# Kernel optimization log

Measured on AMD Instinct MI355X. Metric: run time of the kernel, lower is better.

## Reference

```python
import jax, jax.numpy as jnp
import numpy as np

D_MODEL = 128
N_HEADS = 8
D_K = D_MODEL // N_HEADS
N_NODES = 50000
N_EDGES = 800000


def setup_inputs() -> dict:
    key = jax.random.key(0)
    ks = jax.random.split(key, 8)
    X = jax.random.normal(ks[0], (N_NODES, D_MODEL), dtype=jnp.float32)
    nbr_src = jax.random.randint(ks[1], (N_EDGES,), 0, N_NODES, dtype=jnp.int32)
    nbr_dst = jax.random.randint(ks[2], (N_EDGES,), 0, N_NODES, dtype=jnp.int32)
    s = 1.0 / np.sqrt(D_MODEL)
    W_qkv = jax.random.normal(ks[3], (3 * D_MODEL, D_MODEL), dtype=jnp.float32) * s
    w_bias = jax.random.normal(ks[4], (N_HEADS, D_MODEL), dtype=jnp.float32) * s
    W_gate = jax.random.normal(ks[5], (D_MODEL, D_MODEL), dtype=jnp.float32) * s
    b_gate = jax.random.normal(ks[6], (D_MODEL,), dtype=jnp.float32) * s
    W_o = jax.random.normal(ks[7], (D_MODEL, D_MODEL), dtype=jnp.float32) * s
    return {"X": X, "W_qkv": W_qkv, "w_bias": w_bias, "W_gate": W_gate,
            "b_gate": b_gate, "W_o": W_o, "nbr_src": nbr_src,
            "nbr_dst": nbr_dst, "num_cells": N_NODES}


def segment_softmax(scores, seg, num_segments):
    # scores: [E, H], seg: [E] -> softmax over edges sharing the same seg id
    mx = jax.ops.segment_max(scores, seg, num_segments=num_segments)  # [N, H]
    mx = jnp.where(jnp.isfinite(mx), mx, -1e9)
    exp_s = jnp.exp(scores - mx[seg])
    sm = jax.ops.segment_sum(exp_s, seg, num_segments=num_segments)  # [N, H]
    return exp_s / (sm[seg] + 1e-12)


def reference(X, W_qkv, w_bias, W_gate, b_gate, W_o, nbr_src, nbr_dst, num_cells):
    H, dk = N_HEADS, D_K
    scale = 1.0 / np.sqrt(dk)
    qkv = (X @ W_qkv.T).reshape(-1, 3, H, dk)      # [N, 3, H, dk]
    Q, K, V = qkv[:, 0], qkv[:, 1], qkv[:, 2]
    gate = jax.nn.sigmoid(X @ W_gate.T + b_gate).reshape(-1, H, dk)
    bias = X @ w_bias.T                             # [N, H]
    scores = jnp.einsum('ehd,ehd->eh', Q[nbr_src], K[nbr_dst]) * scale + bias[nbr_src]
    attn = segment_softmax(scores, nbr_src, num_cells)          # [E, H]
    out = jax.ops.segment_sum(attn[:, :, None] * V[nbr_dst], nbr_src,
                              num_segments=num_cells)           # [N, H, dk]
    return (gate * out).reshape(-1, D_MODEL) @ W_o.T
```

## Files before the change

kernel.cpp:

```cpp
#include <hip/hip_runtime.h>
#include <hip/hip_fp16.h>

#define DM 128
#define NHEADS 8
#define MAXDEG 64
#define SROW 136

typedef _Float16 half8 __attribute__((ext_vector_type(8)));
typedef _Float16 half2v __attribute__((ext_vector_type(2)));
typedef float floatx4 __attribute__((ext_vector_type(4)));

union H8 { half8 v; half2v h2[4]; };

__global__ __launch_bounds__(256) void csr_build(
    const int* __restrict__ nsrc, const int* __restrict__ ndst,
    int* __restrict__ cnt, unsigned short* __restrict__ csr_dst, int E) {
  int tid = threadIdx.x;
  int ebase = blockIdx.x * 2048;
  int s[8], d[8];
#pragma unroll
  for (int j = 0; j < 8; j++) {
    int e = ebase + j * 256 + tid;
    s[j] = (e < E) ? nsrc[e] : -1;
    d[j] = (e < E) ? ndst[e] : 0;
  }
#pragma unroll
  for (int j = 0; j < 8; j++) {
    if (s[j] >= 0) {
      int p = atomicAdd(&cnt[s[j]], 1);
      if (p < MAXDEG) csr_dst[(size_t)s[j] * MAXDEG + p] = (unsigned short)d[j];
    }
  }
}

__device__ __forceinline__ void prefetch_B(
    int tid, int c, const float* __restrict__ Wqkv,
    const float* __restrict__ Wgate, const float* __restrict__ wbias,
    float4 pf[4][2]) {
#pragma unroll
  for (int i = 0; i < 4; i++) {
    int u = tid + i * 256;
    int r = u >> 4;
    int cc = (u & 15) * 8;
    int grow = c * 64 + r;
    const float* src = nullptr;
    if (grow < 384)      src = Wqkv + (size_t)grow * 128 + cc;
    else if (grow < 512) src = Wgate + (size_t)(grow - 384) * 128 + cc;
    else if (grow < 520) src = wbias + (size_t)(grow - 512) * 128 + cc;
    if (src) {
      pf[i][0] = ((const float4*)src)[0];
      pf[i][1] = ((const float4*)src)[1];
    } else {
      pf[i][0] = make_float4(0.f, 0.f, 0.f, 0.f);
      pf[i][1] = make_float4(0.f, 0.f, 0.f, 0.f);
    }
  }
}

__global__ __launch_bounds__(256) void proj_gemm(
    const float* __restrict__ X, const float* __restrict__ Wqkv,
    const float* __restrict__ Wgate, const float* __restrict__ wbias,
    const float* __restrict__ b_gate,
    _Float16* __restrict__ Q, _Float16* __restrict__ KV,
    _Float16* __restrict__ gate, float* __restrict__ bias, int M) {
  __shared__ _Float16 As[128 * SROW];
  __shared__ _Float16 Bs[64 * SROW];
  int tid = threadIdx.x;
  int m0 = blockIdx.x * 128;

  float4 pf[4][2];
  prefetch_B(tid, 0, Wqkv, Wgate, wbias, pf);

#pragma unroll
  for (int i = 0; i < 4; i++) {
    int u = tid + i * 256;
    int r = u >> 3;
    int cc = (u & 7) * 16;
    int gr = m0 + r;
    float4 f0, f1, f2, f3;
    if (gr < M) {
      const float4* src = (const float4*)(X + (size_t)gr * 128 + cc);
      f0 = src[0]; f1 = src[1]; f2 = src[2]; f3 = src[3];
    } else {
      f0 = f1 = f2 = f3 = make_float4(0.f, 0.f, 0.f, 0.f);
    }
    half8 h0 = {(_Float16)f0.x, (_Float16)f0.y, (_Float16)f0.z, (_Float16)f0.w,
                (_Float16)f1.x, (_Float16)f1.y, (_Float16)f1.z, (_Float16)f1.w};
    half8 h1 = {(_Float16)f2.x, (_Float16)f2.y, (_Float16)f2.z, (_Float16)f2.w,
                (_Float16)f3.x, (_Float16)f3.y, (_Float16)f3.z, (_Float16)f3.w};
    *(half8*)(As + r * SROW + cc) = h0;
    *(half8*)(As + r * SROW + cc + 8) = h1;
  }

  int wid = tid >> 6, lane = tid & 63;
  int quad = lane >> 4, l16 = lane & 15;
  int mw = wid * 32;

  for (int c = 0; c < 9; c++) {
    __syncthreads();
#pragma unroll
    for (int i = 0; i < 4; i++) {
      int u = tid + i * 256;
      int r = u >> 4;
      int cc = (u & 15) * 8;
      half8 h = {(_Float16)pf[i][0].x, (_Float16)pf[i][0].y,
                 (_Float16)pf[i][0].z, (_Float16)pf[i][0].w,
                 (_Float16)pf[i][1].x, (_Float16)pf[i][1].y,
                 (_Float16)pf[i][1].z, (_Float16)pf[i][1].w};
      *(half8*)(Bs + r * SROW + cc) = h;
    }
    if (c < 8) prefetch_B(tid, c + 1, Wqkv, Wgate, wbias, pf);
    __syncthreads();

    floatx4 acc[2][4] = {};
#pragma unroll
    for (int kc = 0; kc < 4; kc++) {
      int ko = kc * 32 + quad * 8;
      half8 a0 = *(const half8*)(As + (mw + l16) * SROW + ko);
      half8 a1 = *(const half8*)(As + (mw + 16 + l16) * SROW + ko);
      half8 b[4];
#pragma unroll
      for (int ni = 0; ni < 4; ni++)
        b[ni] = *(const half8*)(Bs + (ni * 16 + l16) * SROW + ko);
#pragma unroll
      for (int ni = 0; ni < 4; ni++) {
        acc[0][ni] = __builtin_amdgcn_mfma_f32_16x16x32_f16(a0, b[ni], acc[0][ni], 0, 0, 0);
        acc[1][ni] = __builtin_amdgcn_mfma_f32_16x16x32_f16(a1, b[ni], acc[1][ni], 0, 0, 0);
      }
    }

    if (c == 8) {
      if (l16 < 8) {
#pragma unroll
        for (int mi = 0; mi < 2; mi++)
#pragma unroll
          for (int r = 0; r < 4; r++) {
            int row = m0 + mw + mi * 16 + quad * 4 + r;
            if (row < M) bias[(size_t)row * 8 + l16] = acc[mi][0][r];
          }
      }
    } else {
      int reg = c >> 1;
#pragma unroll
      for (int mi = 0; mi < 2; mi++) {
#pragma unroll
        for (int ni = 0; ni < 4; ni++) {
          int colL = (c & 1) * 64 + ni * 16 + l16;
#pragma unroll
          for (int r = 0; r < 4; r++) {
            int row = m0 + mw + mi * 16 + quad * 4 + r;
            if (row >= M) continue;
            float v = acc[mi][ni][r];
            if (reg == 0)      Q[(size_t)row * 128 + colL] = (_Float16)v;
            else if (reg == 1) KV[(size_t)row * 256 + colL] = (_Float16)v;
            else if (reg == 2) KV[(size_t)row * 256 + 128 + colL] = (_Float16)v;
            else gate[(size_t)row * 128 + colL] =
                   (_Float16)(1.0f / (1.0f + __expf(-(v + b_gate[colL]))));
          }
        }
      }
    }
  }
}

__global__ __launch_bounds__(256) void final_gemm_mfma(
    const _Float16* __restrict__ A, const float* __restrict__ Wo,
    float* __restrict__ C, int M) {
  __shared__ _Float16 As[128 * SROW];
  __shared__ _Float16 Bs[64 * SROW];
  int tid = threadIdx.x;
  int m0 = blockIdx.x * 128, n0 = blockIdx.y * 64;
#pragma unroll
  for (int i = 0; i < 8; i++) {
    int u = tid + i * 256;
    int r = u >> 4;
    int cc = (u & 15) * 8;
    int gr = m0 + r;
    int4 val = make_int4(0, 0, 0, 0);
    if (gr < M) val = *(const int4*)(A + (size_t)gr * 128 + cc);
    *(int4*)(As + r * SROW + cc) = val;
  }
#pragma unroll
  for (int i = 0; i < 4; i++) {
    int u = tid + i * 256;
    int r = u >> 4;
    int cc = (u & 15) * 8;
    const float* src = Wo + (size_t)(n0 + r) * 128 + cc;
    float4 f0 = ((const float4*)src)[0];
    float4 f1 = ((const float4*)src)[1];
    half8 h = {(_Float16)f0.x, (_Float16)f0.y, (_Float16)f0.z, (_Float16)f0.w,
               (_Float16)f1.x, (_Float16)f1.y, (_Float16)f1.z, (_Float16)f1.w};
    *(half8*)(Bs + r * SROW + cc) = h;
  }
  __syncthreads();

  int wid = tid >> 6, lane = tid & 63;
  int quad = lane >> 4, l16 = lane & 15;
  int mw = (wid >> 1) * 64;
  int nw = (wid & 1) * 32;

  floatx4 acc[4][2] = {};
#pragma unroll
  for (int kc = 0; kc < 4; kc++) {
    int ko = kc * 32 + quad * 8;
    half8 a[4], b[2];
#pragma unroll
    for (int mi = 0; mi < 4; mi++)
      a[mi] = *(const half8*)(As + (mw + mi * 16 + l16) * SROW + ko);
#pragma unroll
    for (int ni = 0; ni < 2; ni++)
      b[ni] = *(const half8*)(Bs + (nw + ni * 16 + l16) * SROW + ko);
#pragma unroll
    for (int mi = 0; mi < 4; mi++)
#pragma unroll
      for (int ni = 0; ni < 2; ni++)
        acc[mi][ni] = __builtin_amdgcn_mfma_f32_16x16x32_f16(a[mi], b[ni], acc[mi][ni], 0, 0, 0);
  }
#pragma unroll
  for (int mi = 0; mi < 4; mi++) {
#pragma unroll
    for (int ni = 0; ni < 2; ni++) {
      int col = n0 + nw + ni * 16 + l16;
#pragma unroll
      for (int r = 0; r < 4; r++) {
        int row = m0 + mw + mi * 16 + quad * 4 + r;
        if (row >= M) continue;
        C[(size_t)row * 128 + col] = acc[mi][ni][r];
      }
    }
  }
}

__global__ __launch_bounds__(256) void attn_fused(
    const int* __restrict__ cnt, const unsigned short* __restrict__ csr_dst,
    const _Float16* __restrict__ Q, const _Float16* __restrict__ KV,
    const float* __restrict__ bias, const _Float16* __restrict__ gate,
    _Float16* __restrict__ gated, int N) {
  int wave = threadIdx.x >> 6, lane = threadIdx.x & 63;
  int n = blockIdx.x * 4 + wave;
  if (n >= N) return;
  int deg = cnt[n];
  if (deg > MAXDEG) deg = MAXDEG;
  int qtr = lane >> 4, l16 = lane & 15;
  int ch0 = l16 * 8;

  int dstv = csr_dst[(size_t)n * MAXDEG + lane];

  H8 qu; qu.v = *(const half8*)(Q + (size_t)n * DM + ch0);
  float bias_h = bias[(size_t)n * NHEADS + (l16 >> 1)];

  float acc[8] = {};
  float den = 0.f;
  int iters = (deg + 3) >> 2;

  H8 k0, v0, k1, v1;
  k0.v = half8{}; v0.v = half8{}; k1.v = half8{}; v1.v = half8{};
  bool b0 = false, b1 = false;
  if (0 < iters) {
    int e = qtr;
    b0 = e < deg;
    int d = __shfl(dstv, e);
    d = b0 ? d : 0;
    const _Float16* kvp = KV + (size_t)d * 256 + ch0;
    k0.v = *(const half8*)kvp;
    v0.v = *(const half8*)(kvp + 128);
  }
  if (1 < iters) {
    int e = 4 + qtr;
    b1 = e < deg;
    int d = __shfl(dstv, e);
    d = b1 ? d : 0;
    const _Float16* kvp = KV + (size_t)d * 256 + ch0;
    k1.v = *(const half8*)kvp;
    v1.v = *(const half8*)(kvp + 128);
  }

  for (int it = 0; it < iters; it++) {
    H8 k2, v2;
    k2.v = half8{}; v2.v = half8{};
    bool b2 = false;
    if (it + 2 < iters) {
      int e = (it + 2) * 4 + qtr;
      b2 = e < deg;
      int d = __shfl(dstv, e);
      d = b2 ? d : 0;
      const _Float16* kvp = KV + (size_t)d * 256 + ch0;
      k2.v = *(const half8*)kvp;
      v2.v = *(const half8*)(kvp + 128);
    }
    float p = 0.f;
#pragma unroll
    for (int j = 0; j < 4; j++)
      p = __builtin_amdgcn_fdot2(qu.h2[j], k0.h2[j], p, false);
    p += __shfl_xor(p, 1);
    float w = __expf(p * 0.25f + bias_h);
    if (!b0) w = 0.f;
    den += w;
#pragma unroll
    for (int j = 0; j < 8; j++) acc[j] = fmaf(w, (float)v0.v[j], acc[j]);
    k0 = k1; v0 = v1; b0 = b1;
    k1 = k2; v1 = v2; b1 = b2;
  }
#pragma unroll
  for (int j = 0; j < 8; j++) acc[j] += __shfl_xor(acc[j], 16);
#pragma unroll
  for (int j = 0; j < 8; j++) acc[j] += __shfl_xor(acc[j], 32);
  den += __shfl_xor(den, 16);
  den += __shfl_xor(den, 32);

  if (qtr == 0) {
    float inv = 1.0f / (den + 1e-12f);
    half8 gv = *(const half8*)(gate + (size_t)n * DM + ch0);
    half8 o;
#pragma unroll
    for (int j = 0; j < 8; j++) o[j] = (_Float16)(acc[j] * inv * (float)gv[j]);
    *(half8*)(gated + (size_t)n * DM + ch0) = o;
  }
}

extern "C" void kernel_launch(void* const* d_in, const int* in_sizes, int n_in,
                              void* d_out, int out_size, void* d_ws, size_t ws_size,
                              hipStream_t stream) {
  const float* X     = (const float*)d_in[0];
  const float* Wqkv  = (const float*)d_in[1];
  const float* wbias = (const float*)d_in[2];
  const float* Wgate = (const float*)d_in[3];
  const float* bgate = (const float*)d_in[4];
  const float* Wo    = (const float*)d_in[5];
  const int*   nsrc  = (const int*)d_in[6];
  const int*   ndst  = (const int*)d_in[7];
  int N = in_sizes[0] / 128;
  int E = in_sizes[6];
  float* out = (float*)d_out;

  char* p = (char*)d_ws;
  _Float16* Q16     = (_Float16*)p; p += (size_t)N * 128 * sizeof(_Float16);
  _Float16* KV16    = (_Float16*)p; p += (size_t)N * 256 * sizeof(_Float16);
  _Float16* gate16  = (_Float16*)p; p += (size_t)N * 128 * sizeof(_Float16);
  _Float16* gated16 = (_Float16*)p; p += (size_t)N * 128 * sizeof(_Float16);
  float* bias       = (float*)p;    p += (size_t)N * 8 * sizeof(float);
  int* cnt          = (int*)p;      p += (size_t)N * sizeof(int);
  unsigned short* csr_dst = (unsigned short*)p;
  p += (size_t)N * MAXDEG * sizeof(unsigned short);

  hipMemsetAsync(cnt, 0, (size_t)N * sizeof(int), stream);

  int P = (N + 127) / 128;
  proj_gemm<<<P, 256, 0, stream>>>(X, Wqkv, Wgate, wbias, bgate,
                                   Q16, KV16, gate16, bias, N);

  int C = (E + 2047) / 2048;
  csr_build<<<C, 256, 0, stream>>>(nsrc, ndst, cnt, csr_dst, E);

  attn_fused<<<(N + 3) / 4, 256, 0, stream>>>(cnt, csr_dst, Q16, KV16, bias,
                                              gate16, gated16, N);

  dim3 fg((N + 127) / 128, 2);
  final_gemm_mfma<<<fg, 256, 0, stream>>>(gated16, Wo, out, N);
}
```

Measured before the change: 250.8 us.

## Merge CSR build into projection launch, deepen KV prefetch, use nontemporal accesses

The CSR-building work now runs as extra blocks of the projection GEMM kernel, which removes one launch and lets the atomic scatter overlap with the GEMM. Each CSR block handles four times as many edges. In the attention kernel, the two-deep register prefetch of K/V rows becomes a four-slot rotating buffer, keeping more gathers in flight. Per-node reads and the gated output use nontemporal loads and stores. The deeper buffer raises register pressure, and nontemporal hints may lose cache reuse for data read again later.

```diff
diff --git a/kernel.cpp b/kernel.cpp
--- a/kernel.cpp
+++ b/kernel.cpp
@@ -11,27 +11,6 @@
 typedef float floatx4 __attribute__((ext_vector_type(4)));
 
 union H8 { half8 v; half2v h2[4]; };
-
-__global__ __launch_bounds__(256) void csr_build(
-    const int* __restrict__ nsrc, const int* __restrict__ ndst,
-    int* __restrict__ cnt, unsigned short* __restrict__ csr_dst, int E) {
-  int tid = threadIdx.x;
-  int ebase = blockIdx.x * 2048;
-  int s[8], d[8];
-#pragma unroll
-  for (int j = 0; j < 8; j++) {
-    int e = ebase + j * 256 + tid;
-    s[j] = (e < E) ? nsrc[e] : -1;
-    d[j] = (e < E) ? ndst[e] : 0;
-  }
-#pragma unroll
-  for (int j = 0; j < 8; j++) {
-    if (s[j] >= 0) {
-      int p = atomicAdd(&cnt[s[j]], 1);
-      if (p < MAXDEG) csr_dst[(size_t)s[j] * MAXDEG + p] = (unsigned short)d[j];
-    }
-  }
-}
 
 __device__ __forceinline__ void prefetch_B(
     int tid, int c, const float* __restrict__ Wqkv,
@@ -57,16 +36,42 @@
   }
 }
 
-__global__ __launch_bounds__(256) void proj_gemm(
+__global__ __launch_bounds__(256) void proj_csr(
     const float* __restrict__ X, const float* __restrict__ Wqkv,
     const float* __restrict__ Wgate, const float* __restrict__ wbias,
     const float* __restrict__ b_gate,
+    const int* __restrict__ nsrc, const int* __restrict__ ndst,
+    int* __restrict__ cnt, unsigned short* __restrict__ csr_dst,
     _Float16* __restrict__ Q, _Float16* __restrict__ KV,
-    _Float16* __restrict__ gate, float* __restrict__ bias, int M) {
+    _Float16* __restrict__ gate, float* __restrict__ bias,
+    int M, int E, int P) {
   __shared__ _Float16 As[128 * SROW];
   __shared__ _Float16 Bs[64 * SROW];
   int tid = threadIdx.x;
-  int m0 = blockIdx.x * 128;
+  int bid = blockIdx.x;
+
+  if (bid >= P) {
+    int ebase = (bid - P) * 8192;
+    for (int g = 0; g < 4; g++) {
+      int s[8], d[8];
+#pragma unroll
+      for (int j = 0; j < 8; j++) {
+        int e = ebase + (g * 8 + j) * 256 + tid;
+        s[j] = (e < E) ? __builtin_nontemporal_load(nsrc + e) : -1;
+        d[j] = (e < E) ? __builtin_nontemporal_load(ndst + e) : 0;
+      }
+#pragma unroll
+      for (int j = 0; j < 8; j++) {
+        if (s[j] >= 0) {
+          int p = atomicAdd(&cnt[s[j]], 1);
+          if (p < MAXDEG) csr_dst[(size_t)s[j] * MAXDEG + p] = (unsigned short)d[j];
+        }
+      }
+    }
+    return;
+  }
+
+  int m0 = bid * 128;
 
   float4 pf[4][2];
   prefetch_B(tid, 0, Wqkv, Wgate, wbias, pf);
@@ -239,68 +244,64 @@
   int wave = threadIdx.x >> 6, lane = threadIdx.x & 63;
   int n = blockIdx.x * 4 + wave;
   if (n >= N) return;
-  int deg = cnt[n];
+  int deg = __builtin_nontemporal_load(cnt + n);
   if (deg > MAXDEG) deg = MAXDEG;
   int qtr = lane >> 4, l16 = lane & 15;
   int ch0 = l16 * 8;
 
-  int dstv = csr_dst[(size_t)n * MAXDEG + lane];
-
-  H8 qu; qu.v = *(const half8*)(Q + (size_t)n * DM + ch0);
-  float bias_h = bias[(size_t)n * NHEADS + (l16 >> 1)];
+  int dstv = (int)__builtin_nontemporal_load(csr_dst + (size_t)n * MAXDEG + lane);
+
+  H8 qu; qu.v = __builtin_nontemporal_load((const half8*)(Q + (size_t)n * DM + ch0));
+  float bias_h = __builtin_nontemporal_load(bias + (size_t)n * NHEADS + (l16 >> 1));
 
   float acc[8] = {};
   float den = 0.f;
   int iters = (deg + 3) >> 2;
 
-  H8 k0, v0, k1, v1;
-  k0.v = half8{}; v0.v = half8{}; k1.v = half8{}; v1.v = half8{};
-  bool b0 = false, b1 = false;
-  if (0 < iters) {
-    int e = qtr;
-    b0 = e < deg;
-    int d = __shfl(dstv, e);
-    d = b0 ? d : 0;
-    const _Float16* kvp = KV + (size_t)d * 256 + ch0;
-    k0.v = *(const half8*)kvp;
-    v0.v = *(const half8*)(kvp + 128);
-  }
-  if (1 < iters) {
-    int e = 4 + qtr;
-    b1 = e < deg;
-    int d = __shfl(dstv, e);
-    d = b1 ? d : 0;
-    const _Float16* kvp = KV + (size_t)d * 256 + ch0;
-    k1.v = *(const half8*)kvp;
-    v1.v = *(const half8*)(kvp + 128);
-  }
-
-  for (int it = 0; it < iters; it++) {
-    H8 k2, v2;
-    k2.v = half8{}; v2.v = half8{};
-    bool b2 = false;
-    if (it + 2 < iters) {
-      int e = (it + 2) * 4 + qtr;
-      b2 = e < deg;
+  H8 kb[4], vb[4];
+  bool bb[4];
+#pragma unroll
+  for (int j = 0; j < 4; j++) {
+    bb[j] = false;
+    kb[j].v = half8{}; vb[j].v = half8{};
+    if (j < iters) {
+      int e = j * 4 + qtr;
+      bb[j] = e < deg;
       int d = __shfl(dstv, e);
-      d = b2 ? d : 0;
+      d = bb[j] ? d : 0;
       const _Float16* kvp = KV + (size_t)d * 256 + ch0;
-      k2.v = *(const half8*)kvp;
-      v2.v = *(const half8*)(kvp + 128);
-    }
-    float p = 0.f;
-#pragma unroll
-    for (int j = 0; j < 4; j++)
-      p = __builtin_amdgcn_fdot2(qu.h2[j], k0.h2[j], p, false);
-    p += __shfl_xor(p, 1);
-    float w = __expf(p * 0.25f + bias_h);
-    if (!b0) w = 0.f;
-    den += w;
-#pragma unroll
-    for (int j = 0; j < 8; j++) acc[j] = fmaf(w, (float)v0.v[j], acc[j]);
-    k0 = k1; v0 = v1; b0 = b1;
-    k1 = k2; v1 = v2; b1 = b2;
-  }
+      kb[j].v = *(const half8*)kvp;
+      vb[j].v = *(const half8*)(kvp + 128);
+    }
+  }
+
+  for (int base = 0; base < iters; base += 4) {
+#pragma unroll
+    for (int j = 0; j < 4; j++) {
+      float p = 0.f;
+#pragma unroll
+      for (int t = 0; t < 4; t++)
+        p = __builtin_amdgcn_fdot2(qu.h2[t], kb[j].h2[t], p, false);
+      p += __shfl_xor(p, 1);
+      float w = __expf(p * 0.25f + bias_h);
+      if (!bb[j]) w = 0.f;
+      den += w;
+#pragma unroll
+      for (int t = 0; t < 8; t++) acc[t] = fmaf(w, (float)vb[j].v[t], acc[t]);
+      int idx = base + 4 + j;
+      bb[j] = false;
+      if (idx < iters) {
+        int e = idx * 4 + qtr;
+        bb[j] = e < deg;
+        int d = __shfl(dstv, e);
+        d = bb[j] ? d : 0;
+        const _Float16* kvp = KV + (size_t)d * 256 + ch0;
+        kb[j].v = *(const half8*)kvp;
+        vb[j].v = *(const half8*)(kvp + 128);
+      }
+    }
+  }
+
 #pragma unroll
   for (int j = 0; j < 8; j++) acc[j] += __shfl_xor(acc[j], 16);
 #pragma unroll
@@ -310,11 +311,11 @@
 
   if (qtr == 0) {
     float inv = 1.0f / (den + 1e-12f);
-    half8 gv = *(const half8*)(gate + (size_t)n * DM + ch0);
+    half8 gv = __builtin_nontemporal_load((const half8*)(gate + (size_t)n * DM + ch0));
     half8 o;
 #pragma unroll
     for (int j = 0; j < 8; j++) o[j] = (_Float16)(acc[j] * inv * (float)gv[j]);
-    *(half8*)(gated + (size_t)n * DM + ch0) = o;
+    __builtin_nontemporal_store(o, (half8*)(gated + (size_t)n * DM + ch0));
   }
 }
 
@@ -346,11 +347,9 @@
   hipMemsetAsync(cnt, 0, (size_t)N * sizeof(int), stream);
 
   int P = (N + 127) / 128;
-  proj_gemm<<<P, 256, 0, stream>>>(X, Wqkv, Wgate, wbias, bgate,
-                                   Q16, KV16, gate16, bias, N);
-
-  int C = (E + 2047) / 2048;
-  csr_build<<<C, 256, 0, stream>>>(nsrc, ndst, cnt, csr_dst, E);
+  int C = (E + 8191) / 8192;
+  proj_csr<<<P + C, 256, 0, stream>>>(X, Wqkv, Wgate, wbias, bgate, nsrc, ndst,
+                                      cnt, csr_dst, Q16, KV16, gate16, bias, N, E, P);
 
   attn_fused<<<(N + 3) / 4, 256, 0, stream>>>(cnt, csr_dst, Q16, KV16, bias,
                                               gate16, gated16, N);
```

New measurement: 230.8 us. 8.0% less time.
